# Optimization experiments

Hardware: AMD Instinct MI355X
Metric: run time of the kernel (lower is better)

## Reference

```python
import jax, jax.numpy as jnp
import numpy as np
import math

STATE_SHAPE = (128, 128, 64)
BATCH = 8
EPS = 1e-8
STATE_SIZE = math.prod(STATE_SHAPE)


def setup_inputs() -> dict:
    key = jax.random.key(0)
    ks = jax.random.split(key, 9)
    inp = {
        "x_real": jax.random.normal(ks[0], (BATCH, *STATE_SHAPE), dtype=jnp.float32),
        "x_imag": jax.random.normal(ks[1], (BATCH, *STATE_SHAPE), dtype=jnp.float32),
    }
    for m, dim in enumerate(STATE_SHAPE):
        inp[f"w{m}_real"] = 0.02 * jax.random.normal(ks[2 + 2 * m], (dim, dim), dtype=jnp.float32)
        inp[f"w{m}_imag"] = 0.02 * jax.random.normal(ks[3 + 2 * m], (dim, dim), dtype=jnp.float32)
    inp["log_tau"] = jnp.zeros((1,), dtype=jnp.float32)  # log(tau_init=1.0)
    return inp


def _mode_step(x, W, mode, tau):
    # x: (B, *STATE_SHAPE) complex; W: (d, d) complex
    B = x.shape[0]
    d = x.shape[mode + 1]
    # unfold: move mode axis to position 1, flatten the rest -> (B, d, rest)
    u = jnp.moveaxis(x, mode + 1, 1)
    perm_shape = u.shape
    u = u.reshape(B, d, -1)
    left = jnp.einsum('ij,bjk->bik', W, u)           # (B, d, rest)
    score = left @ jnp.swapaxes(u, -1, -2)           # (B, d, d) complex
    scale = tau * jnp.sqrt(jnp.float32(STATE_SIZE) / jnp.float32(d))
    mag = jnp.abs(score)
    routing = jax.nn.softmax(mag / scale, axis=-1)
    safe_mag = jnp.maximum(mag, EPS)
    phase = jnp.where(mag > EPS, score / safe_mag, jnp.ones_like(score))
    matrix = routing.astype(score.dtype) * phase     # (B, d, d) complex
    mixed = matrix @ u                               # (B, d, rest)
    # fold back
    return jnp.moveaxis(mixed.reshape(perm_shape), 1, mode + 1)


def reference(x_real, x_imag, w0_real, w0_imag, w1_real, w1_imag, w2_real, w2_imag, log_tau):
    x = jax.lax.complex(x_real, x_imag)
    Ws = [
        jax.lax.complex(w0_real, w0_imag),
        jax.lax.complex(w1_real, w1_imag),
        jax.lax.complex(w2_real, w2_imag),
    ]
    tau = jnp.maximum(jnp.exp(log_tau[0]), EPS)
    mixed = x
    for mode in range(len(STATE_SHAPE)):
        mixed = _mode_step(mixed, Ws[mode], mode, tau)
    # return real/imag stacked as float32 for harness comparability
    return jnp.stack([mixed.real, mixed.imag], axis=0)
```

## Files before the change

### kernel.cpp

```cpp
#include <hip/hip_runtime.h>
#include <math.h>

#define BATCH 8
#define SSIZE 1048576


typedef short sh8 __attribute__((ext_vector_type(8)));
typedef float f32x4 __attribute__((ext_vector_type(4)));

#define MFMA16(a, b, c) __builtin_amdgcn_mfma_f32_16x16x32_bf16((a), (b), (c), 0, 0, 0)

__device__ __forceinline__ unsigned short bf_rne(float x) {
    unsigned u = __float_as_uint(x);
    unsigned r = u + 0x7fffu + ((u >> 16) & 1u);
    return (unsigned short)(r >> 16);
}

__device__ __forceinline__ void split1(float x, unsigned short &h, unsigned short &l) {
    h = bf_rne(x);
    float hf = __uint_as_float((unsigned)h << 16);
    l = bf_rne(x - hf);
}

__device__ __forceinline__ void split2(float a, float b, unsigned &hh, unsigned &ll) {
    unsigned short ha = bf_rne(a), hb = bf_rne(b);
    hh = (unsigned)ha | ((unsigned)hb << 16);
    float ra = a - __uint_as_float((unsigned)ha << 16);
    float rb = b - __uint_as_float((unsigned)hb << 16);
    ll = (unsigned)bf_rne(ra) | ((unsigned)bf_rne(rb) << 16);
}

__device__ __forceinline__ float f4c(const float4 &v, int c) {
    return c == 0 ? v.x : c == 1 ? v.y : c == 2 ? v.z : v.w;
}

__device__ __forceinline__ sh8 ldfrag(const unsigned short *pl, int row, int kg) {
    const int idx = (row * 32 + kg * 8) ^ ((row & 3) << 3);
    return *(const sh8 *)(pl + idx);
}

__device__ __forceinline__ sh8 ldfrag40(const unsigned short *pl, int row, int kg) {
    return *(const sh8 *)(pl + row * 40 + kg * 8);
}

template<int NS, int PERB>
__global__ __launch_bounds__(256)
void reduce_kernel(const float4* __restrict__ in, float4* __restrict__ out) {
    const int gid = blockIdx.x * blockDim.x + threadIdx.x;
    const int b = gid / PERB, r = gid - b * PERB;
    const float4* p = in + (size_t)b * NS * PERB + r;
    float4 a = p[0];
    #pragma unroll 8
    for (int s = 1; s < NS; s++) {
        const float4 v = p[(size_t)s * PERB];
        a.x += v.x; a.y += v.y; a.z += v.z; a.w += v.w;
    }
    out[gid] = a;
}

template<int SI_, int KL2_, int SKH_>
__global__ __launch_bounds__(256, 3)
void gram_mfma_kernel(const float* __restrict__ srcR, const float* __restrict__ srcI,
                      float* __restrict__ Gp, int kPerBlock)
{
    const int tile = blockIdx.x;
    const int it = (tile == 2) ? 64 : 0;
    const int jt = (tile == 0) ? 0 : 64;
    const bool diag = (it == jt);
    const int b  = blockIdx.z;
    const int k0 = blockIdx.y * kPerBlock;

    const int t    = threadIdx.x;
    const int lane = t & 63;
    const int wave = t >> 6;
    const int wr = wave & 1, wc = wave >> 1;

    __shared__ unsigned short SA[4][2048];
    __shared__ unsigned short SB[4][2048];

    const sh8 SGN = {(short)0x8000, (short)0x8000, (short)0x8000, (short)0x8000,
                     (short)0x8000, (short)0x8000, (short)0x8000, (short)0x8000};

    f32x4 gr[2][2], gi[2][2];
    const f32x4 z4 = {0.f, 0.f, 0.f, 0.f};
    #pragma unroll
    for (int x = 0; x < 2; x++)
        #pragma unroll
        for (int y = 0; y < 2; y++) { gr[x][y] = z4; gi[x][y] = z4; }

    const size_t boff = (size_t)b * SSIZE;
    const int nT = kPerBlock >> 5;

    const int kq   = t & 7;
    const int row2 = t >> 3;

    const int frow = lane & 15;
    const int kg   = lane >> 4;

    #define GADDR(ii, k) (boff + (size_t)(ii) * SI_ + \
        (size_t)((k) >> KL2_) * SKH_ + (size_t)((k) & ((1 << KL2_) - 1)))

    for (int kt = 0; kt < nT; kt++) {
        const int kb = k0 + kt * 32;
        #pragma unroll
        for (int m = 0; m < 2; m++) {
            const int row = row2 + 32 * m;
            const int idx = (row * 32 + kq * 4) ^ ((row & 3) << 3);
            {
                const size_t off = GADDR(it + row, kb + kq * 4);
                const float4 R = *(const float4*)(srcR + off);
                const float4 I = *(const float4*)(srcI + off);
                ushort4 rh, rl, ih, il;
                split1(R.x, rh.x, rl.x); split1(R.y, rh.y, rl.y);
                split1(R.z, rh.z, rl.z); split1(R.w, rh.w, rl.w);
                split1(I.x, ih.x, il.x); split1(I.y, ih.y, il.y);
                split1(I.z, ih.z, il.z); split1(I.w, ih.w, il.w);
                *(ushort4*)&SA[0][idx] = rh;
                *(ushort4*)&SA[1][idx] = rl;
                *(ushort4*)&SA[2][idx] = ih;
                *(ushort4*)&SA[3][idx] = il;
            }
            if (!diag) {
                const size_t off = GADDR(jt + row, kb + kq * 4);
                const float4 R = *(const float4*)(srcR + off);
                const float4 I = *(const float4*)(srcI + off);
                ushort4 rh, rl, ih, il;
                split1(R.x, rh.x, rl.x); split1(R.y, rh.y, rl.y);
                split1(R.z, rh.z, rl.z); split1(R.w, rh.w, rl.w);
                split1(I.x, ih.x, il.x); split1(I.y, ih.y, il.y);
                split1(I.z, ih.z, il.z); split1(I.w, ih.w, il.w);
                *(ushort4*)&SB[0][idx] = rh;
                *(ushort4*)&SB[1][idx] = rl;
                *(ushort4*)&SB[2][idx] = ih;
                *(ushort4*)&SB[3][idx] = il;
            }
        }
        __syncthreads();

        unsigned short (*BP)[2048] = diag ? SA : SB;

        sh8 a[2][4], na[2][2], bfr[2][4];
        #pragma unroll
        for (int s = 0; s < 2; s++) {
            const int row = wr * 32 + s * 16 + frow;
            #pragma unroll
            for (int p = 0; p < 4; p++) a[s][p] = ldfrag(&SA[p][0], row, kg);
            na[s][0] = a[s][2] ^ SGN;
            na[s][1] = a[s][3] ^ SGN;
        }
        #pragma unroll
        for (int s = 0; s < 2; s++) {
            const int row = wc * 32 + s * 16 + frow;
            #pragma unroll
            for (int p = 0; p < 4; p++) bfr[s][p] = ldfrag(&BP[p][0], row, kg);
        }

        #pragma unroll
        for (int sr = 0; sr < 2; sr++) {
            #pragma unroll
            for (int sc = 0; sc < 2; sc++) {
                f32x4 r = gr[sr][sc], q = gi[sr][sc];
                r = MFMA16(a[sr][0],  bfr[sc][0], r);
                r = MFMA16(a[sr][0],  bfr[sc][1], r);
                r = MFMA16(a[sr][1],  bfr[sc][0], r);
                r = MFMA16(na[sr][0], bfr[sc][2], r);
                r = MFMA16(na[sr][0], bfr[sc][3], r);
                r = MFMA16(na[sr][1], bfr[sc][2], r);
                q = MFMA16(a[sr][0],  bfr[sc][2], q);
                q = MFMA16(a[sr][0],  bfr[sc][3], q);
                q = MFMA16(a[sr][1],  bfr[sc][2], q);
                q = MFMA16(a[sr][2],  bfr[sc][0], q);
                q = MFMA16(a[sr][2],  bfr[sc][1], q);
                q = MFMA16(a[sr][3],  bfr[sc][0], q);
                gr[sr][sc] = r; gi[sr][sc] = q;
            }
        }
        __syncthreads();
    }
    #undef GADDR

    float* Gb = Gp + ((size_t)b * gridDim.y + blockIdx.y) * (128 * 128 * 2);
    const int rb   = (lane >> 4) * 4;
    const int jcol = lane & 15;
    #pragma unroll
    for (int sr = 0; sr < 2; sr++)
        #pragma unroll
        for (int sc = 0; sc < 2; sc++)
            #pragma unroll
            for (int r = 0; r < 4; r++) {
                const int i = it + wr * 32 + sr * 16 + rb + r;
                const int j = jt + wc * 32 + sc * 16 + jcol;
                const float vr = gr[sr][sc][r], vi = gi[sr][sc][r];
                *(float2*)&Gb[(i * 128 + j) * 2] = make_float2(vr, vi);
                if (!diag)
                    *(float2*)&Gb[(j * 128 + i) * 2] = make_float2(vr, vi);
            }
}

__global__ __launch_bounds__(256, 4)
void gram64_mfma_kernel(const float* __restrict__ srcR, const float* __restrict__ srcI,
                        float* __restrict__ Gp, int kPerBlock)
{
    const int b  = blockIdx.y;
    const int k0 = blockIdx.x * kPerBlock;

    const int t    = threadIdx.x;
    const int lane = t & 63;
    const int wave = t >> 6;
    const int wr = wave & 1, wc = wave >> 1;

    __shared__ unsigned short SA[4][2048];

    const sh8 SGN = {(short)0x8000, (short)0x8000, (short)0x8000, (short)0x8000,
                     (short)0x8000, (short)0x8000, (short)0x8000, (short)0x8000};

    f32x4 gr[2][2], gi[2][2];
    const f32x4 z4 = {0.f, 0.f, 0.f, 0.f};
    #pragma unroll
    for (int x = 0; x < 2; x++)
        #pragma unroll
        for (int y = 0; y < 2; y++) { gr[x][y] = z4; gi[x][y] = z4; }

    const size_t boff = (size_t)b * SSIZE;
    const int nT = kPerBlock >> 5;

    const int kp = t & 15;
    const int i0 = (t >> 4) * 4;

    const int frow = lane & 15;
    const int kg   = lane >> 4;

    for (int kt = 0; kt < nT; kt++) {
        const int kb = k0 + kt * 32;
        const int ke = kb + 2 * kp;
        const int ko = ke + 1;
        const size_t offE = boff + (size_t)(ke & 127) * 64 + (size_t)(ke >> 7) * 8192 + i0;
        const size_t offO = boff + (size_t)(ko & 127) * 64 + (size_t)(ko >> 7) * 8192 + i0;
        const float4 R0 = *(const float4*)(srcR + offE);
        const float4 I0 = *(const float4*)(srcI + offE);
        const float4 R1 = *(const float4*)(srcR + offO);
        const float4 I1 = *(const float4*)(srcI + offO);
        const int kw = 2 * kp;
        #pragma unroll
        for (int c = 0; c < 4; c++) {
            const int i   = i0 + c;
            const int idx = (i * 32 + kw) ^ ((i & 3) << 3);
            unsigned short h0, l0, h1, l1;
            split1(f4c(R0, c), h0, l0);
            split1(f4c(R1, c), h1, l1);
            *(ushort2*)&SA[0][idx] = make_ushort2(h0, h1);
            *(ushort2*)&SA[1][idx] = make_ushort2(l0, l1);
            split1(f4c(I0, c), h0, l0);
            split1(f4c(I1, c), h1, l1);
            *(ushort2*)&SA[2][idx] = make_ushort2(h0, h1);
            *(ushort2*)&SA[3][idx] = make_ushort2(l0, l1);
        }
        __syncthreads();

        sh8 a[2][4], na[2][2], bfr[2][4];
        #pragma unroll
        for (int s = 0; s < 2; s++) {
            const int row = wr * 32 + s * 16 + frow;
            #pragma unroll
            for (int p = 0; p < 4; p++) a[s][p] = ldfrag(&SA[p][0], row, kg);
            na[s][0] = a[s][2] ^ SGN;
            na[s][1] = a[s][3] ^ SGN;
        }
        #pragma unroll
        for (int s = 0; s < 2; s++) {
            const int row = wc * 32 + s * 16 + frow;
            #pragma unroll
            for (int p = 0; p < 4; p++) bfr[s][p] = ldfrag(&SA[p][0], row, kg);
        }

        #pragma unroll
        for (int sr = 0; sr < 2; sr++) {
            #pragma unroll
            for (int sc = 0; sc < 2; sc++) {
                f32x4 r = gr[sr][sc], q = gi[sr][sc];
                r = MFMA16(a[sr][0],  bfr[sc][0], r);
                r = MFMA16(a[sr][0],  bfr[sc][1], r);
                r = MFMA16(a[sr][1],  bfr[sc][0], r);
                r = MFMA16(na[sr][0], bfr[sc][2], r);
                r = MFMA16(na[sr][0], bfr[sc][3], r);
                r = MFMA16(na[sr][1], bfr[sc][2], r);
                q = MFMA16(a[sr][0],  bfr[sc][2], q);
                q = MFMA16(a[sr][0],  bfr[sc][3], q);
                q = MFMA16(a[sr][1],  bfr[sc][2], q);
                q = MFMA16(a[sr][2],  bfr[sc][0], q);
                q = MFMA16(a[sr][2],  bfr[sc][1], q);
                q = MFMA16(a[sr][3],  bfr[sc][0], q);
                gr[sr][sc] = r; gi[sr][sc] = q;
            }
        }
        __syncthreads();
    }

    float* Gb = Gp + ((size_t)b * gridDim.x + blockIdx.x) * (64 * 64 * 2);
    const int rb   = (lane >> 4) * 4;
    const int jcol = lane & 15;
    #pragma unroll
    for (int sr = 0; sr < 2; sr++)
        #pragma unroll
        for (int sc = 0; sc < 2; sc++)
            #pragma unroll
            for (int r = 0; r < 4; r++) {
                const int i = wr * 32 + sr * 16 + rb + r;
                const int j = wc * 32 + sc * 16 + jcol;
                *(float2*)&Gb[(i * 64 + j) * 2] = make_float2(gr[sr][sc][r], gi[sr][sc][r]);
            }
}

__global__ __launch_bounds__(128)
void score_kernel(const float* __restrict__ G,
                  const float* __restrict__ Wre, const float* __restrict__ Wim,
                  const float* __restrict__ log_tau,
                  unsigned short* __restrict__ Mout, int d)
{
    const int b = blockIdx.y;
    const int i = blockIdx.x;
    const int j = threadIdx.x;

    const float2* Gb = (const float2*)G + (size_t)b * d * d;

    float sre = 0.f, sim = 0.f;
    for (int l = 0; l < d; l++) {
        float wr = Wre[i * d + l];
        float wi = Wim[i * d + l];
        float2 g = Gb[l * d + j];
        sre = fmaf(wr, g.x, sre);
        sre = fmaf(-wi, g.y, sre);
        sim = fmaf(wr, g.y, sim);
        sim = fmaf(wi, g.x, sim);
    }

    float mag = sqrtf(sre * sre + sim * sim);
    float tau = fmaxf(expf(log_tau[0]), 1e-8f);
    float scale = tau * sqrtf((float)SSIZE / (float)d);
    float mval = mag / scale;

    __shared__ float red[128];
    red[j] = mval;
    __syncthreads();
    for (int s = d >> 1; s > 0; s >>= 1) {
        if (j < s) red[j] = fmaxf(red[j], red[j + s]);
        __syncthreads();
    }
    float mx = red[0];
    __syncthreads();
    float e = expf(mval - mx);
    red[j] = e;
    __syncthreads();
    for (int s = d >> 1; s > 0; s >>= 1) {
        if (j < s) red[j] += red[j + s];
        __syncthreads();
    }
    float routing = e / red[0];

    float safe = fmaxf(mag, 1e-8f);
    float pre, pim;
    if (mag > 1e-8f) { pre = sre / safe; pim = sim / safe; }
    else             { pre = 1.f;       pim = 0.f; }

    const float mr = routing * pre;
    const float mi = routing * pim;
    const size_t dd = (size_t)d * d;
    unsigned short h, l;
    split1(mr, h, l);
    Mout[((size_t)b * 4 + 0) * dd + i * d + j] = h;
    Mout[((size_t)b * 4 + 1) * dd + i * d + j] = l;
    split1(mi, h, l);
    Mout[((size_t)b * 4 + 2) * dd + i * d + j] = h;
    Mout[((size_t)b * 4 + 3) * dd + i * d + j] = l;
}

template<int SI_, int KL2_, int SKH_>
__global__ __launch_bounds__(256, 4)
void mix128_mfma_kernel(const float* __restrict__ srcR, const float* __restrict__ srcI,
                        const unsigned short* __restrict__ Mp,
                        float* __restrict__ dstR, float* __restrict__ dstI)
{
    const int kb0 = blockIdx.x << 6;
    const int it  = blockIdx.y << 6;
    const int b   = blockIdx.z;

    const int t    = threadIdx.x;
    const int lane = t & 63;
    const int wave = t >> 6;
    const int wr = wave & 1, wc = wave >> 1;

    __shared__ unsigned short UP[4][2560];
    __shared__ unsigned short MP[4][2560];

    const sh8 SGN = {(short)0x8000, (short)0x8000, (short)0x8000, (short)0x8000,
                     (short)0x8000, (short)0x8000, (short)0x8000, (short)0x8000};

    f32x4 gr[2][2], gi[2][2];
    const f32x4 z4 = {0.f, 0.f, 0.f, 0.f};
    #pragma unroll
    for (int x = 0; x < 2; x++)
        #pragma unroll
        for (int y = 0; y < 2; y++) { gr[x][y] = z4; gi[x][y] = z4; }

    const size_t boff = (size_t)b * SSIZE;
    const unsigned short* Mb = Mp + (size_t)b * 4 * 16384;

    #define GADDR(jj, k) (boff + (size_t)(jj) * SI_ + \
        (size_t)((k) >> KL2_) * SKH_ + (size_t)((k) & ((1 << KL2_) - 1)))

    const int ujp = t & 15;
    const int uq  = t >> 4;
    const int mi  = t >> 2;
    const int mj8 = (t & 3) * 8;

    const int frow = lane & 15;
    const int kg   = lane >> 4;

    for (int jt = 0; jt < 4; jt++) {
        const int jb = jt * 32;
        {
            const int src = (it + mi) * 128 + jb + mj8;
            const int idx = mi * 40 + mj8;
            #pragma unroll
            for (int p = 0; p < 4; p++)
                *(uint4*)&MP[p][idx] = *(const uint4*)&Mb[p * 16384 + src];
        }
        {
            const int j0 = 2 * ujp;
            const size_t o0 = GADDR(jb + j0,     kb0 + 4 * uq);
            const size_t o1 = GADDR(jb + j0 + 1, kb0 + 4 * uq);
            const float4 R0 = *(const float4*)(srcR + o0);
            const float4 R1 = *(const float4*)(srcR + o1);
            const float4 I0 = *(const float4*)(srcI + o0);
            const float4 I1 = *(const float4*)(srcI + o1);
            #pragma unroll
            for (int c = 0; c < 4; c++) {
                const int kc  = 4 * uq + c;
                const int idx = kc * 40 + j0;
                unsigned hh, ll;
                split2(f4c(R0, c), f4c(R1, c), hh, ll);
                *(unsigned*)&UP[0][idx] = hh;
                *(unsigned*)&UP[1][idx] = ll;
                split2(f4c(I0, c), f4c(I1, c), hh, ll);
                *(unsigned*)&UP[2][idx] = hh;
                *(unsigned*)&UP[3][idx] = ll;
            }
        }
        __syncthreads();

        sh8 a[2][4], na[2][2], bfr[2][4];
        #pragma unroll
        for (int s = 0; s < 2; s++) {
            const int row = wr * 32 + s * 16 + frow;
            #pragma unroll
            for (int p = 0; p < 4; p++) a[s][p] = ldfrag40(&UP[p][0], row, kg);
            na[s][0] = a[s][2] ^ SGN;
            na[s][1] = a[s][3] ^ SGN;
        }
        #pragma unroll
        for (int s = 0; s < 2; s++) {
            const int row = wc * 32 + s * 16 + frow;
            #pragma unroll
            for (int p = 0; p < 4; p++) bfr[s][p] = ldfrag40(&MP[p][0], row, kg);
        }

        #pragma unroll
        for (int sr = 0; sr < 2; sr++) {
            #pragma unroll
            for (int sc = 0; sc < 2; sc++) {
                f32x4 r = gr[sr][sc], q = gi[sr][sc];
                r = MFMA16(a[sr][0],  bfr[sc][0], r);
                r = MFMA16(a[sr][0],  bfr[sc][1], r);
                r = MFMA16(a[sr][1],  bfr[sc][0], r);
                r = MFMA16(na[sr][0], bfr[sc][2], r);
                r = MFMA16(na[sr][0], bfr[sc][3], r);
                r = MFMA16(na[sr][1], bfr[sc][2], r);
                q = MFMA16(a[sr][0],  bfr[sc][2], q);
                q = MFMA16(a[sr][0],  bfr[sc][3], q);
                q = MFMA16(a[sr][1],  bfr[sc][2], q);
                q = MFMA16(a[sr][2],  bfr[sc][0], q);
                q = MFMA16(a[sr][2],  bfr[sc][1], q);
                q = MFMA16(a[sr][3],  bfr[sc][0], q);
                gr[sr][sc] = r; gi[sr][sc] = q;
            }
        }
        __syncthreads();
    }

    #pragma unroll
    for (int sr = 0; sr < 2; sr++)
        #pragma unroll
        for (int sc = 0; sc < 2; sc++) {
            const int k = kb0 + wr * 32 + sr * 16 + 4 * (lane >> 4);
            const int i = it  + wc * 32 + sc * 16 + (lane & 15);
            const size_t o = boff + (size_t)i * SI_ +
                (size_t)(k >> KL2_) * SKH_ + (size_t)(k & ((1 << KL2_) - 1));
            *(float4*)(dstR + o) = make_float4(gr[sr][sc][0], gr[sr][sc][1],
                                               gr[sr][sc][2], gr[sr][sc][3]);
            *(float4*)(dstI + o) = make_float4(gi[sr][sc][0], gi[sr][sc][1],
                                               gi[sr][sc][2], gi[sr][sc][3]);
        }
    #undef GADDR
}

__global__ __launch_bounds__(256, 4)
void mix64_mfma_kernel(const float* __restrict__ srcR, const float* __restrict__ srcI,
                       const unsigned short* __restrict__ Mp,
                       float* __restrict__ dstR, float* __restrict__ dstI)
{
    const int kb0 = blockIdx.x << 6;
    const int b   = blockIdx.y;

    const int t    = threadIdx.x;
    const int lane = t & 63;
    const int wave = t >> 6;
    const int wr = wave & 1, wc = wave >> 1;

    __shared__ unsigned short UP[4][2560];
    __shared__ unsigned short MP[4][2560];

    const sh8 SGN = {(short)0x8000, (short)0x8000, (short)0x8000, (short)0x8000,
                     (short)0x8000, (short)0x8000, (short)0x8000, (short)0x8000};

    f32x4 gr[2][2], gi[2][2];
    const f32x4 z4 = {0.f, 0.f, 0.f, 0.f};
    #pragma unroll
    for (int x = 0; x < 2; x++)
        #pragma unroll
        for (int y = 0; y < 2; y++) { gr[x][y] = z4; gi[x][y] = z4; }

    const size_t boff  = (size_t)b * SSIZE;
    const unsigned short* Mb = Mp + (size_t)b * 4 * 4096;
    const size_t koffb = (size_t)(kb0 & 127) * 64 + (size_t)(kb0 >> 7) * 8192;

    const int mi  = t >> 2;
    const int mj8 = (t & 3) * 8;
    const int ujq = t & 7;
    const int ukc = t >> 3;

    const int frow = lane & 15;
    const int kg   = lane >> 4;

    for (int jt = 0; jt < 2; jt++) {
        const int jb = jt * 32;
        {
            const int src = mi * 64 + jb + mj8;
            const int idx = mi * 40 + mj8;
            #pragma unroll
            for (int p = 0; p < 4; p++)
                *(uint4*)&MP[p][idx] = *(const uint4*)&Mb[p * 4096 + src];
        }
        #pragma unroll
        for (int m = 0; m < 2; m++) {
            const int kc = ukc + 32 * m;
            const size_t o = boff + koffb + (size_t)kc * 64 + jb + 4 * ujq;
            const float4 R = *(const float4*)(srcR + o);
            const float4 I = *(const float4*)(srcI + o);
            const int idx = kc * 40 + 4 * ujq;
            unsigned h0, l0, h1, l1;
            split2(R.x, R.y, h0, l0); split2(R.z, R.w, h1, l1);
            *(uint2*)&UP[0][idx] = make_uint2(h0, h1);
            *(uint2*)&UP[1][idx] = make_uint2(l0, l1);
            split2(I.x, I.y, h0, l0); split2(I.z, I.w, h1, l1);
            *(uint2*)&UP[2][idx] = make_uint2(h0, h1);
            *(uint2*)&UP[3][idx] = make_uint2(l0, l1);
        }
        __syncthreads();

        sh8 a[2][4], na[2][2], bfr[2][4];
        #pragma unroll
        for (int s = 0; s < 2; s++) {
            const int row = wr * 32 + s * 16 + frow;
            #pragma unroll
            for (int p = 0; p < 4; p++) a[s][p] = ldfrag40(&MP[p][0], row, kg);
            na[s][0] = a[s][2] ^ SGN;
            na[s][1] = a[s][3] ^ SGN;
        }
        #pragma unroll
        for (int s = 0; s < 2; s++) {
            const int row = wc * 32 + s * 16 + frow;
            #pragma unroll
            for (int p = 0; p < 4; p++) bfr[s][p] = ldfrag40(&UP[p][0], row, kg);
        }

        #pragma unroll
        for (int sr = 0; sr < 2; sr++) {
            #pragma unroll
            for (int sc = 0; sc < 2; sc++) {
                f32x4 r = gr[sr][sc], q = gi[sr][sc];
                r = MFMA16(a[sr][0],  bfr[sc][0], r);
                r = MFMA16(a[sr][0],  bfr[sc][1], r);
                r = MFMA16(a[sr][1],  bfr[sc][0], r);
                r = MFMA16(na[sr][0], bfr[sc][2], r);
                r = MFMA16(na[sr][0], bfr[sc][3], r);
                r = MFMA16(na[sr][1], bfr[sc][2], r);
                q = MFMA16(a[sr][0],  bfr[sc][2], q);
                q = MFMA16(a[sr][0],  bfr[sc][3], q);
                q = MFMA16(a[sr][1],  bfr[sc][2], q);
                q = MFMA16(a[sr][2],  bfr[sc][0], q);
                q = MFMA16(a[sr][2],  bfr[sc][1], q);
                q = MFMA16(a[sr][3],  bfr[sc][0], q);
                gr[sr][sc] = r; gi[sr][sc] = q;
            }
        }
        __syncthreads();
    }

    #pragma unroll
    for (int sr = 0; sr < 2; sr++)
        #pragma unroll
        for (int sc = 0; sc < 2; sc++) {
            const int i  = wr * 32 + sr * 16 + 4 * (lane >> 4);
            const int kc = wc * 32 + sc * 16 + (lane & 15);
            const size_t o = boff + koffb + (size_t)kc * 64 + i;
            *(float4*)(dstR + o) = make_float4(gr[sr][sc][0], gr[sr][sc][1],
                                               gr[sr][sc][2], gr[sr][sc][3]);
            *(float4*)(dstI + o) = make_float4(gi[sr][sc][0], gi[sr][sc][1],
                                               gi[sr][sc][2], gi[sr][sc][3]);
        }
}

extern "C" void kernel_launch(void* const* d_in, const int* in_sizes, int n_in,
                              void* d_out, int out_size, void* d_ws, size_t ws_size,
                              hipStream_t stream)
{
    const float* xr  = (const float*)d_in[0];
    const float* xi  = (const float*)d_in[1];
    const float* w0r = (const float*)d_in[2];
    const float* w0i = (const float*)d_in[3];
    const float* w1r = (const float*)d_in[4];
    const float* w1i = (const float*)d_in[5];
    const float* w2r = (const float*)d_in[6];
    const float* w2i = (const float*)d_in[7];
    const float* lt  = (const float*)d_in[8];

    float* outR = (float*)d_out;
    float* outI = outR + (size_t)BATCH * SSIZE;

    float*  wsR = (float*)d_ws;
    float*  wsI = wsR + (size_t)BATCH * SSIZE;
    float*  Gf  = wsI + (size_t)BATCH * SSIZE;
    unsigned short* Mp = (unsigned short*)(Gf + (size_t)BATCH * 128 * 128 * 2);


    gram_mfma_kernel<8192, 13, 0><<<dim3(3, 32, BATCH), 256, 0, stream>>>(xr, xi, outR, 256);
    reduce_kernel<32, 8192><<<dim3(256), 256, 0, stream>>>((const float4*)outR, (float4*)Gf);
    score_kernel<<<dim3(128, BATCH), 128, 0, stream>>>(Gf, w0r, w0i, lt, Mp, 128);
    mix128_mfma_kernel<8192, 13, 0><<<dim3(128, 2, BATCH), 256, 0, stream>>>(xr, xi, Mp, outR, outI);

    gram_mfma_kernel<64, 6, 8192><<<dim3(3, 32, BATCH), 256, 0, stream>>>(outR, outI, wsR, 256);
    reduce_kernel<32, 8192><<<dim3(256), 256, 0, stream>>>((const float4*)wsR, (float4*)Gf);
    score_kernel<<<dim3(128, BATCH), 128, 0, stream>>>(Gf, w1r, w1i, lt, Mp, 128);
    mix128_mfma_kernel<64, 6, 8192><<<dim3(128, 2, BATCH), 256, 0, stream>>>(outR, outI, Mp, wsR, wsI);

    gram64_mfma_kernel<<<dim3(128, BATCH), 256, 0, stream>>>(wsR, wsI, outR, 128);
    reduce_kernel<128, 2048><<<dim3(64), 256, 0, stream>>>((const float4*)outR, (float4*)Gf);
    score_kernel<<<dim3(64, BATCH), 64, 0, stream>>>(Gf, w2r, w2i, lt, Mp, 64);
    mix64_mfma_kernel<<<dim3(256, BATCH), 256, 0, stream>>>(wsR, wsI, Mp, outR, outI);
}
```

Measured before the change: 422.0 us.

## Prefetch next k-tile global loads into registers before MFMA compute

In all four GEMM-style kernels, the global loads for the next k/j tile are now issued right after the barrier, into registers, so they overlap with the MFMA work on the current tile. The loaded values are split to bf16 and stored to shared memory at the top of the next iteration. This hides global memory latency behind compute, at the cost of extra registers per thread, which may lower occupancy.

```diff
diff --git a/kernel.cpp b/kernel.cpp
--- a/kernel.cpp
+++ b/kernel.cpp
@@ -100,35 +100,45 @@
     #define GADDR(ii, k) (boff + (size_t)(ii) * SI_ + \
         (size_t)((k) >> KL2_) * SKH_ + (size_t)((k) & ((1 << KL2_) - 1)))
 
+    float4 pAR[2], pAI[2], pBR[2], pBI[2];
+    auto loadk = [&](int kb) {
+        #pragma unroll
+        for (int m = 0; m < 2; m++) {
+            const int row = row2 + 32 * m;
+            const size_t offA = GADDR(it + row, kb + kq * 4);
+            pAR[m] = *(const float4*)(srcR + offA);
+            pAI[m] = *(const float4*)(srcI + offA);
+            if (!diag) {
+                const size_t offB = GADDR(jt + row, kb + kq * 4);
+                pBR[m] = *(const float4*)(srcR + offB);
+                pBI[m] = *(const float4*)(srcI + offB);
+            }
+        }
+    };
+
+    loadk(k0);
     for (int kt = 0; kt < nT; kt++) {
-        const int kb = k0 + kt * 32;
         #pragma unroll
         for (int m = 0; m < 2; m++) {
             const int row = row2 + 32 * m;
             const int idx = (row * 32 + kq * 4) ^ ((row & 3) << 3);
             {
-                const size_t off = GADDR(it + row, kb + kq * 4);
-                const float4 R = *(const float4*)(srcR + off);
-                const float4 I = *(const float4*)(srcI + off);
                 ushort4 rh, rl, ih, il;
-                split1(R.x, rh.x, rl.x); split1(R.y, rh.y, rl.y);
-                split1(R.z, rh.z, rl.z); split1(R.w, rh.w, rl.w);
-                split1(I.x, ih.x, il.x); split1(I.y, ih.y, il.y);
-                split1(I.z, ih.z, il.z); split1(I.w, ih.w, il.w);
+                split1(pAR[m].x, rh.x, rl.x); split1(pAR[m].y, rh.y, rl.y);
+                split1(pAR[m].z, rh.z, rl.z); split1(pAR[m].w, rh.w, rl.w);
+                split1(pAI[m].x, ih.x, il.x); split1(pAI[m].y, ih.y, il.y);
+                split1(pAI[m].z, ih.z, il.z); split1(pAI[m].w, ih.w, il.w);
                 *(ushort4*)&SA[0][idx] = rh;
                 *(ushort4*)&SA[1][idx] = rl;
                 *(ushort4*)&SA[2][idx] = ih;
                 *(ushort4*)&SA[3][idx] = il;
             }
             if (!diag) {
-                const size_t off = GADDR(jt + row, kb + kq * 4);
-                const float4 R = *(const float4*)(srcR + off);
-                const float4 I = *(const float4*)(srcI + off);
                 ushort4 rh, rl, ih, il;
-                split1(R.x, rh.x, rl.x); split1(R.y, rh.y, rl.y);
-                split1(R.z, rh.z, rl.z); split1(R.w, rh.w, rl.w);
-                split1(I.x, ih.x, il.x); split1(I.y, ih.y, il.y);
-                split1(I.z, ih.z, il.z); split1(I.w, ih.w, il.w);
+                split1(pBR[m].x, rh.x, rl.x); split1(pBR[m].y, rh.y, rl.y);
+                split1(pBR[m].z, rh.z, rl.z); split1(pBR[m].w, rh.w, rl.w);
+                split1(pBI[m].x, ih.x, il.x); split1(pBI[m].y, ih.y, il.y);
+                split1(pBI[m].z, ih.z, il.z); split1(pBI[m].w, ih.w, il.w);
                 *(ushort4*)&SB[0][idx] = rh;
                 *(ushort4*)&SB[1][idx] = rl;
                 *(ushort4*)&SB[2][idx] = ih;
@@ -136,6 +146,8 @@
             }
         }
         __syncthreads();
+
+        if (kt + 1 < nT) loadk(k0 + (kt + 1) * 32);
 
         unsigned short (*BP)[2048] = diag ? SA : SB;
 
@@ -230,32 +242,38 @@
     const int frow = lane & 15;
     const int kg   = lane >> 4;
 
-    for (int kt = 0; kt < nT; kt++) {
-        const int kb = k0 + kt * 32;
+    float4 qR[2], qI[2];
+    auto loadk = [&](int kb) {
         const int ke = kb + 2 * kp;
         const int ko = ke + 1;
         const size_t offE = boff + (size_t)(ke & 127) * 64 + (size_t)(ke >> 7) * 8192 + i0;
         const size_t offO = boff + (size_t)(ko & 127) * 64 + (size_t)(ko >> 7) * 8192 + i0;
-        const float4 R0 = *(const float4*)(srcR + offE);
-        const float4 I0 = *(const float4*)(srcI + offE);
-        const float4 R1 = *(const float4*)(srcR + offO);
-        const float4 I1 = *(const float4*)(srcI + offO);
+        qR[0] = *(const float4*)(srcR + offE);
+        qI[0] = *(const float4*)(srcI + offE);
+        qR[1] = *(const float4*)(srcR + offO);
+        qI[1] = *(const float4*)(srcI + offO);
+    };
+
+    loadk(k0);
+    for (int kt = 0; kt < nT; kt++) {
         const int kw = 2 * kp;
         #pragma unroll
         for (int c = 0; c < 4; c++) {
             const int i   = i0 + c;
             const int idx = (i * 32 + kw) ^ ((i & 3) << 3);
             unsigned short h0, l0, h1, l1;
-            split1(f4c(R0, c), h0, l0);
-            split1(f4c(R1, c), h1, l1);
+            split1(f4c(qR[0], c), h0, l0);
+            split1(f4c(qR[1], c), h1, l1);
             *(ushort2*)&SA[0][idx] = make_ushort2(h0, h1);
             *(ushort2*)&SA[1][idx] = make_ushort2(l0, l1);
-            split1(f4c(I0, c), h0, l0);
-            split1(f4c(I1, c), h1, l1);
+            split1(f4c(qI[0], c), h0, l0);
+            split1(f4c(qI[1], c), h1, l1);
             *(ushort2*)&SA[2][idx] = make_ushort2(h0, h1);
             *(ushort2*)&SA[3][idx] = make_ushort2(l0, l1);
         }
         __syncthreads();
+
+        if (kt + 1 < nT) loadk(k0 + (kt + 1) * 32);
 
         sh8 a[2][4], na[2][2], bfr[2][4];
         #pragma unroll
@@ -416,37 +434,46 @@
     const int frow = lane & 15;
     const int kg   = lane >> 4;
 
+    uint4 pM[4];
+    float4 pR0, pR1, pI0, pI1;
+    auto loadjt = [&](int jb) {
+        const int src = (it + mi) * 128 + jb + mj8;
+        #pragma unroll
+        for (int p = 0; p < 4; p++) pM[p] = *(const uint4*)&Mb[p * 16384 + src];
+        const int j0 = 2 * ujp;
+        const size_t o0 = GADDR(jb + j0,     kb0 + 4 * uq);
+        const size_t o1 = GADDR(jb + j0 + 1, kb0 + 4 * uq);
+        pR0 = *(const float4*)(srcR + o0);
+        pR1 = *(const float4*)(srcR + o1);
+        pI0 = *(const float4*)(srcI + o0);
+        pI1 = *(const float4*)(srcI + o1);
+    };
+
+    loadjt(0);
     for (int jt = 0; jt < 4; jt++) {
-        const int jb = jt * 32;
         {
-            const int src = (it + mi) * 128 + jb + mj8;
             const int idx = mi * 40 + mj8;
             #pragma unroll
-            for (int p = 0; p < 4; p++)
-                *(uint4*)&MP[p][idx] = *(const uint4*)&Mb[p * 16384 + src];
+            for (int p = 0; p < 4; p++) *(uint4*)&MP[p][idx] = pM[p];
         }
         {
             const int j0 = 2 * ujp;
-            const size_t o0 = GADDR(jb + j0,     kb0 + 4 * uq);
-            const size_t o1 = GADDR(jb + j0 + 1, kb0 + 4 * uq);
-            const float4 R0 = *(const float4*)(srcR + o0);
-            const float4 R1 = *(const float4*)(srcR + o1);
-            const float4 I0 = *(const float4*)(srcI + o0);
-            const float4 I1 = *(const float4*)(srcI + o1);
             #pragma unroll
             for (int c = 0; c < 4; c++) {
                 const int kc  = 4 * uq + c;
                 const int idx = kc * 40 + j0;
                 unsigned hh, ll;
-                split2(f4c(R0, c), f4c(R1, c), hh, ll);
+                split2(f4c(pR0, c), f4c(pR1, c), hh, ll);
                 *(unsigned*)&UP[0][idx] = hh;
                 *(unsigned*)&UP[1][idx] = ll;
-                split2(f4c(I0, c), f4c(I1, c), hh, ll);
+                split2(f4c(pI0, c), f4c(pI1, c), hh, ll);
                 *(unsigned*)&UP[2][idx] = hh;
                 *(unsigned*)&UP[3][idx] = ll;
             }
         }
         __syncthreads();
+
+        if (jt + 1 < 4) loadjt((jt + 1) * 32);
 
         sh8 a[2][4], na[2][2], bfr[2][4];
         #pragma unroll
@@ -541,31 +568,43 @@
     const int frow = lane & 15;
     const int kg   = lane >> 4;
 
-    for (int jt = 0; jt < 2; jt++) {
-        const int jb = jt * 32;
-        {
-            const int src = mi * 64 + jb + mj8;
-            const int idx = mi * 40 + mj8;
-            #pragma unroll
-            for (int p = 0; p < 4; p++)
-                *(uint4*)&MP[p][idx] = *(const uint4*)&Mb[p * 4096 + src];
-        }
+    uint4 pM[4];
+    float4 pR[2], pI[2];
+    auto loadjt = [&](int jb) {
+        const int src = mi * 64 + jb + mj8;
+        #pragma unroll
+        for (int p = 0; p < 4; p++) pM[p] = *(const uint4*)&Mb[p * 4096 + src];
         #pragma unroll
         for (int m = 0; m < 2; m++) {
             const int kc = ukc + 32 * m;
             const size_t o = boff + koffb + (size_t)kc * 64 + jb + 4 * ujq;
-            const float4 R = *(const float4*)(srcR + o);
-            const float4 I = *(const float4*)(srcI + o);
+            pR[m] = *(const float4*)(srcR + o);
+            pI[m] = *(const float4*)(srcI + o);
+        }
+    };
+
+    loadjt(0);
+    for (int jt = 0; jt < 2; jt++) {
+        {
+            const int idx = mi * 40 + mj8;
+            #pragma unroll
+            for (int p = 0; p < 4; p++) *(uint4*)&MP[p][idx] = pM[p];
+        }
+        #pragma unroll
+        for (int m = 0; m < 2; m++) {
+            const int kc = ukc + 32 * m;
             const int idx = kc * 40 + 4 * ujq;
             unsigned h0, l0, h1, l1;
-            split2(R.x, R.y, h0, l0); split2(R.z, R.w, h1, l1);
+            split2(pR[m].x, pR[m].y, h0, l0); split2(pR[m].z, pR[m].w, h1, l1);
             *(uint2*)&UP[0][idx] = make_uint2(h0, h1);
             *(uint2*)&UP[1][idx] = make_uint2(l0, l1);
-            split2(I.x, I.y, h0, l0); split2(I.z, I.w, h1, l1);
+            split2(pI[m].x, pI[m].y, h0, l0); split2(pI[m].z, pI[m].w, h1, l1);
             *(uint2*)&UP[2][idx] = make_uint2(h0, h1);
             *(uint2*)&UP[3][idx] = make_uint2(l0, l1);
         }
         __syncthreads();
+
+        if (jt + 1 < 2) loadjt((jt + 1) * 32);
 
         sh8 a[2][4], na[2][2], bfr[2][4];
         #pragma unroll
```

New measurement: 459.4 us. +8.9%, slower.
